# Optimization experiments

Measured on AMD Instinct MI355X. Metric: run time of the kernel, lower is better.

Reference implementation:

```python
import jax, jax.numpy as jnp
import numpy as np

T, IO, H, M = 8192, 32, 256, 4  # timesteps, io_width, hidden_width, max ponder steps
EPS = 0.01  # ACT halting epsilon


def setup_inputs() -> dict:
    key = jax.random.key(0)
    ks = jax.random.split(key, 8)
    sc = 0.05
    return {
        "x": jax.random.normal(ks[0], (T, IO), jnp.float32),
        "h0": jnp.zeros((H,), jnp.float32),                       # act1_h initial state
        "Wp": jax.random.normal(ks[1], (H, IO), jnp.float32) * sc,  # input_processing Linear
        "bp": jnp.zeros((H,), jnp.float32),
        "Wx": jax.random.normal(ks[2], (H, H + 1), jnp.float32) * sc,  # ACT cell input weights (+1 first-step flag)
        "Ws": jax.random.normal(ks[3], (H, H), jnp.float32) * sc,      # ACT cell recurrent weights
        "b": jnp.zeros((H,), jnp.float32),
        "wh": jax.random.normal(ks[4], (H,), jnp.float32) * sc,        # halting unit
        "bh": jnp.float32(1.0),
        "Wo": jax.random.normal(ks[5], (IO, H), jnp.float32) * sc,     # ACT output projection
        "bo": jnp.zeros((IO,), jnp.float32),
    }


def reference(x, h0, Wp, bp, Wx, Ws, b, wh, bh, Wo, bo):
    # Faithful translation: per-timestep loop (lax.scan) over the sequence; each step
    # runs input_processing then an ACT (Graves) ponder loop with max M=4 steps.
    # io_noise is identity in eval mode. attention_beam_width=1 => line == current point.
    T_ = x.shape[0]

    def step(carry, x_t):
        h, pc = carry
        lin1 = Wp @ x_t + bp  # [H]
        s = h
        cum = jnp.float32(0.0)
        acc_s = jnp.zeros_like(h)
        acc_y = jnp.zeros_like(bo)
        n_up = jnp.float32(0.0)
        rem = jnp.float32(0.0)
        still = jnp.bool_(True)
        for n in range(M):  # fixed small ponder loop, masked ACT halting
            flag = jnp.full((1,), 1.0 if n == 0 else 0.0, lin1.dtype)
            inp = jnp.concatenate([lin1, flag])  # [H+1]
            s = jnp.tanh(Wx @ inp + Ws @ s + b)
            p = jax.nn.sigmoid(wh @ s + bh)
            halt = (cum + p > 1.0 - EPS) | (n == M - 1)
            w = jnp.where(still, jnp.where(halt, 1.0 - cum, p), 0.0)
            acc_s = acc_s + w * s
            acc_y = acc_y + w * (Wo @ s + bo)
            rem = rem + jnp.where(still & halt, 1.0 - cum, 0.0)
            n_up = n_up + jnp.where(still, 1.0, 0.0)
            cum = cum + w
            still = still & jnp.logical_not(halt)
        ponder = n_up + rem  # N(t) + R(t)
        pc = (pc + ponder) / jnp.float32(T_)  # matches the in-loop division in the original forward
        return (acc_s, pc), acc_y

    (_, pc), ys = jax.lax.scan(step, (h0, jnp.float32(0.0)), x)
    return ys, pc
```

## Files before the change

### kernel.cpp

```cpp
#include <hip/hip_runtime.h>


#define T_  8192
#define IO_ 32
#define H_  256

typedef __attribute__((ext_vector_type(2))) float v2f;

template<int CTRL>
__device__ __forceinline__ float dpp_addf(float x) {
    int xi = __builtin_bit_cast(int, x);
    int d = __builtin_amdgcn_update_dpp(xi, xi, CTRL, 0xF, 0xF, false);
    return x + __builtin_bit_cast(float, d);
}
template<int CTRL>
__device__ __forceinline__ float dpp_get(float x) {
    int xi = __builtin_bit_cast(int, x);
    int d = __builtin_amdgcn_update_dpp(xi, xi, CTRL, 0xF, 0xF, false);
    return __builtin_bit_cast(float, d);
}
__device__ __forceinline__ void bar_lds() {
    asm volatile("s_waitcnt lgkmcnt(0)\n\ts_barrier" ::: "memory");
    __builtin_amdgcn_sched_barrier(0);
}

__device__ __forceinline__ float mv_reduce(const v2f (&wt)[8][8], const v2f (&sc)[8]) {
    float v[8];
    #pragma unroll
    for (int k = 0; k < 8; ++k) {
        v2f a = wt[k][0] * sc[0];
        #pragma unroll
        for (int q = 1; q < 8; ++q) a += wt[k][q] * sc[q];
        v[k] = a.x + a.y;
    }
    #pragma unroll
    for (int k = 0; k < 8; ++k) v[k] = dpp_addf<0x128>(v[k]);
    v[0] += dpp_get<0x124>(v[4]);
    v[1] += dpp_get<0x124>(v[5]);
    v[2] += dpp_get<0x124>(v[6]);
    v[3] += dpp_get<0x124>(v[7]);
    v[0] += dpp_get<0x121>(v[1]);
    v[0] += dpp_get<0x122>(v[2]);
    v[0] += dpp_get<0x123>(v[3]);
    return v[0];
}

__global__ void k_prep(const float* __restrict__ Wx,
                       const float* __restrict__ Wp,
                       const float* __restrict__ bp,
                       const float* __restrict__ b,
                       float* __restrict__ WxpT, float* __restrict__ cvec) {
    int h = blockIdx.x;
    int t = threadIdx.x;
    __shared__ float wxrow[H_];
    for (int j = t; j < H_; j += 64) wxrow[j] = Wx[h * (H_ + 1) + j];
    __syncthreads();
    if (t < IO_) {
        float acc = 0.0f;
        for (int j = 0; j < H_; ++j) acc += wxrow[j] * Wp[j * IO_ + t];
        WxpT[t * H_ + h] = acc;
    } else if (t == IO_) {
        float acc = b[h];
        for (int j = 0; j < H_; ++j) acc += wxrow[j] * bp[j];
        cvec[h] = acc;
    }
}

__global__ void k_u(const float* __restrict__ x,
                    const float* __restrict__ WxpT,
                    const float* __restrict__ cvec,
                    float* __restrict__ U) {
    int t0 = blockIdx.x * 8;
    int tid = threadIdx.x;
    __shared__ float xsf[8 * IO_];
    xsf[tid] = x[(size_t)t0 * IO_ + tid];
    __syncthreads();
    int h = tid;
    float base = cvec[h];
    const float L2E2 = 2.8853900817779268f;
    for (int tt = 0; tt < 8; ++tt) {
        float acc = base;
        #pragma unroll
        for (int io = 0; io < IO_; ++io)
            acc += WxpT[io * H_ + h] * xsf[tt * IO_ + io];
        U[(size_t)(t0 + tt) * H_ + h] = acc * L2E2;
    }
}

__global__ __launch_bounds__(512, 2) void act_chain(
    const float* __restrict__ Ws,
    const float* __restrict__ Wx,
    const float* __restrict__ wh,
    const float* __restrict__ bh1,
    const float* __restrict__ h0,
    float* __restrict__ UAcc,
    float* __restrict__ cumArr,
    float* __restrict__ pc_out)
{
    __shared__ __align__(16) float sbuf[2][320];
    __shared__ __align__(16) float plds[2][8];

    const int tid = threadIdx.x;
    const int w   = tid >> 6;
    const int l   = tid & 63;
    const int m   = l & 15;
    const int rbase = w * 32 + ((l >> 4) & 3) * 8;
    const int r_own = rbase + (m & 7);
    const int swidx = (r_own >> 4) * 20 + (r_own & 15);
    const bool pub  = (l & 8) == 0;

    const float L2E  = 1.4426950408889634f;
    const float L2E2 = 2.8853900817779268f;

    v2f wt[8][8];
    #pragma unroll
    for (int k = 0; k < 8; ++k) {
        const int rk = rbase + ((k + m) & 7);
        const float4* s4 = (const float4*)(Ws + (size_t)rk * H_ + m * 16);
        #pragma unroll
        for (int q = 0; q < 4; ++q) {
            float4 f = s4[q];
            wt[k][2 * q]     = (v2f){f.x * L2E2, f.y * L2E2};
            wt[k][2 * q + 1] = (v2f){f.z * L2E2, f.w * L2E2};
        }
    }

    const float wlf = Wx[(size_t)r_own * (H_ + 1) + H_] * L2E2;
    const float whp = wh[r_own] * (-L2E);
    const float bhp = -bh1[0] * L2E;
    const float thresh = 0.99f;

    float zh;
    {
        v2f sc[8];
        const float4* hp = (const float4*)(h0 + m * 16);
        #pragma unroll
        for (int q = 0; q < 4; ++q) {
            float4 f = hp[q];
            sc[2 * q]     = (v2f){f.x, f.y};
            sc[2 * q + 1] = (v2f){f.z, f.w};
        }
        zh = mv_reduce(wt, sc);
    }

    float pc = 0.0f;
    float un_cur = UAcc[r_own];
    float u0_cur = un_cur + wlf;

    auto round = [&](int WB, int PP, float in, float& z, float& p) -> float {
        float e = __builtin_amdgcn_exp2f(in);
        float s = __builtin_fmaf(-2.0f, __builtin_amdgcn_rcpf(e + 1.0f), 1.0f);
        if (pub) sbuf[WB][swidx] = s;
        float part = whp * s;
        part = dpp_addf<0x121>(part);
        part = dpp_addf<0x122>(part);
        part = dpp_addf<0x124>(part);
        part = dpp_addf<0x142>(part);
        part = dpp_addf<0x143>(part);
        if (l == 63) plds[PP][w] = part;
        bar_lds();
        const float4* sp = (const float4*)(&sbuf[WB][m * 20]);
        float4 f0 = sp[0], f1 = sp[1], f2 = sp[2], f3 = sp[3];
        const float4* pr = (const float4*)(&plds[PP][0]);
        float4 qa = pr[0], qb = pr[1];
        v2f sc[8] = {{f0.x, f0.y}, {f0.z, f0.w}, {f1.x, f1.y}, {f1.z, f1.w},
                     {f2.x, f2.y}, {f2.z, f2.w}, {f3.x, f3.y}, {f3.z, f3.w}};
        z = mv_reduce(wt, sc);
        float dot = ((qa.x + qa.y) + (qa.z + qa.w)) +
                    ((qb.x + qb.y) + (qb.z + qb.w));
        p = __builtin_amdgcn_rcpf(1.0f + __builtin_amdgcn_exp2f(dot + bhp));
        return s;
    };

    #pragma unroll 1
    for (int t = 0; t < T_; ++t) {
        const int tn = (t + 1 < T_) ? t + 1 : t;
        const float un_nxt = UAcc[(size_t)tn * H_ + r_own];

        float z0, p0, z1, p1;
        float s0 = round(0, 0, zh + u0_cur, z0, p0);
        float s1 = round(1, 1, z0 + un_cur, z1, p1);

        bool  halt0  = p0 > thresh;
        float w0     = halt0 ? 1.0f : p0;
        bool  still1 = !halt0;
        float cum1   = w0;
        bool  halt1  = (cum1 + p1 > thresh);
        float w1     = still1 ? (halt1 ? 1.0f - cum1 : p1) : 0.0f;
        float accs   = __builtin_fmaf(w1, s1, w0 * s0);
        float zacc   = __builtin_fmaf(w1, z1, w0 * z0);
        float cum    = cum1 + w1;
        float nup    = still1 ? 2.0f : 1.0f;
        float rem    = halt0 ? 1.0f : (halt1 ? 1.0f - cum1 : 0.0f);

        if (still1 && !halt1) {
            float z2, p2, z3, p3;
            float s2 = round(0, 0, z1 + un_cur, z2, p2);
            bool  halt2 = (cum + p2 > thresh);
            float w2    = halt2 ? 1.0f - cum : p2;
            float rem2  = halt2 ? 1.0f - cum : 0.0f;
            accs = __builtin_fmaf(w2, s2, accs);
            zacc = __builtin_fmaf(w2, z2, zacc);
            float cum3  = cum + w2;
            bool  still3 = !halt2;
            float s3 = round(1, 1, z2 + un_cur, z3, p3);
            float w3 = still3 ? (1.0f - cum3) : 0.0f;
            accs = __builtin_fmaf(w3, s3, accs);
            zacc = __builtin_fmaf(w3, z3, zacc);
            rem  = rem2 + w3;
            cum  = cum3 + w3;
            nup  = still3 ? 4.0f : 3.0f;
        }

        pc = (pc + nup + rem) * (1.0f / (float)T_);
        zh = zacc;
        if (pub) UAcc[(size_t)t * H_ + r_own] = accs;
        if (tid == 0) cumArr[t] = cum;
        un_cur = un_nxt;
        u0_cur = un_nxt + wlf;
    }
    if (tid == 0) pc_out[0] = pc;
}

__global__ void k_out(const float* __restrict__ AccS,
                      const float* __restrict__ Wo,
                      const float* __restrict__ bo,
                      const float* __restrict__ cumArr,
                      float* __restrict__ ys) {
    int t0 = blockIdx.x * 8;
    int tid = threadIdx.x;
    __shared__ float wo[IO_ * 257];
    __shared__ float as[8 * 260];
    for (int i = tid; i < IO_ * H_; i += 256) {
        int o = i / H_, h = i % H_;
        wo[o * 257 + h] = Wo[i];
    }
    for (int i = tid; i < 8 * H_; i += 256) {
        int tt = i / H_, h = i % H_;
        as[tt * 260 + h] = AccS[(size_t)t0 * H_ + i];
    }
    __syncthreads();
    int tt = tid >> 5, o = tid & 31;
    float acc = cumArr[t0 + tt] * bo[o];
    #pragma unroll 4
    for (int h = 0; h < H_; ++h) acc += wo[o * 257 + h] * as[tt * 260 + h];
    ys[(size_t)(t0 + tt) * IO_ + o] = acc;
}

extern "C" void kernel_launch(void* const* d_in, const int* in_sizes, int n_in,
                              void* d_out, int out_size, void* d_ws, size_t ws_size,
                              hipStream_t stream) {
    const float* x  = (const float*)d_in[0];
    const float* h0 = (const float*)d_in[1];
    const float* Wp = (const float*)d_in[2];
    const float* bp = (const float*)d_in[3];
    const float* Wx = (const float*)d_in[4];
    const float* Ws = (const float*)d_in[5];
    const float* b  = (const float*)d_in[6];
    const float* wh = (const float*)d_in[7];
    const float* bh = (const float*)d_in[8];
    const float* Wo = (const float*)d_in[9];
    const float* bo = (const float*)d_in[10];
    float* out = (float*)d_out;

    char* ws = (char*)d_ws;
    float* WxpT = (float*)ws;
    float* cvec = (float*)(ws + 32768);
    float* cumA = (float*)(ws + 33792);
    float* UAcc = (float*)(ws + 66560);

    k_prep<<<H_, 64, 0, stream>>>(Wx, Wp, bp, b, WxpT, cvec);
    k_u<<<T_ / 8, 256, 0, stream>>>(x, WxpT, cvec, UAcc);
    act_chain<<<1, 512, 0, stream>>>(Ws, Wx, wh, bh, h0, UAcc, cumA,
                                     out + (size_t)T_ * IO_);
    k_out<<<T_ / 8, 256, 0, stream>>>(UAcc, Wo, bo, cumA, out);
}
```

Before: 12.87 ms.

## Remap recurrent matvec to 2 rows x 4 column-chunks per lane

Changes how the Ws recurrent matvec is split across the 512 threads. Each lane now holds two full rows over a 64-column chunk, four lanes cover a row, and the reduction needs only two DPP adds instead of the 8-row rotated layout with a longer DPP tree. Each lane reads its 64 state values straight from LDS as float4s. This aims to shorten the reduction on the serial per-step critical path, at the cost of 64 LDS floats per lane per round instead of 16, a different padding layout, and a pair of tanh values computed per lane.

Result: faster. 12.00 ms (-6.8%).

```diff
diff --git a/kernel.cpp b/kernel.cpp
--- a/kernel.cpp
+++ b/kernel.cpp
@@ -13,36 +13,9 @@
     int d = __builtin_amdgcn_update_dpp(xi, xi, CTRL, 0xF, 0xF, false);
     return x + __builtin_bit_cast(float, d);
 }
-template<int CTRL>
-__device__ __forceinline__ float dpp_get(float x) {
-    int xi = __builtin_bit_cast(int, x);
-    int d = __builtin_amdgcn_update_dpp(xi, xi, CTRL, 0xF, 0xF, false);
-    return __builtin_bit_cast(float, d);
-}
 __device__ __forceinline__ void bar_lds() {
     asm volatile("s_waitcnt lgkmcnt(0)\n\ts_barrier" ::: "memory");
     __builtin_amdgcn_sched_barrier(0);
-}
-
-__device__ __forceinline__ float mv_reduce(const v2f (&wt)[8][8], const v2f (&sc)[8]) {
-    float v[8];
-    #pragma unroll
-    for (int k = 0; k < 8; ++k) {
-        v2f a = wt[k][0] * sc[0];
-        #pragma unroll
-        for (int q = 1; q < 8; ++q) a += wt[k][q] * sc[q];
-        v[k] = a.x + a.y;
-    }
-    #pragma unroll
-    for (int k = 0; k < 8; ++k) v[k] = dpp_addf<0x128>(v[k]);
-    v[0] += dpp_get<0x124>(v[4]);
-    v[1] += dpp_get<0x124>(v[5]);
-    v[2] += dpp_get<0x124>(v[6]);
-    v[3] += dpp_get<0x124>(v[7]);
-    v[0] += dpp_get<0x121>(v[1]);
-    v[0] += dpp_get<0x122>(v[2]);
-    v[0] += dpp_get<0x123>(v[3]);
-    return v[0];
 }
 
 __global__ void k_prep(const float* __restrict__ Wx,
@@ -97,89 +70,105 @@
     float* __restrict__ cumArr,
     float* __restrict__ pc_out)
 {
-    __shared__ __align__(16) float sbuf[2][320];
+    __shared__ __align__(16) float sbuf[2][4 * 68];
     __shared__ __align__(16) float plds[2][8];
 
     const int tid = threadIdx.x;
     const int w   = tid >> 6;
     const int l   = tid & 63;
-    const int m   = l & 15;
-    const int rbase = w * 32 + ((l >> 4) & 3) * 8;
-    const int r_own = rbase + (m & 7);
-    const int swidx = (r_own >> 4) * 20 + (r_own & 15);
-    const bool pub  = (l & 8) == 0;
+    const int rg  = l >> 2;
+    const int c   = l & 3;
+    const int rowbase = w * 32 + rg * 2;
+    const int schunk  = rowbase >> 6;
+    const int soff    = rowbase & 63;
 
     const float L2E  = 1.4426950408889634f;
     const float L2E2 = 2.8853900817779268f;
 
-    v2f wt[8][8];
+    v2f wt[2][32];
     #pragma unroll
-    for (int k = 0; k < 8; ++k) {
-        const int rk = rbase + ((k + m) & 7);
-        const float4* s4 = (const float4*)(Ws + (size_t)rk * H_ + m * 16);
-        #pragma unroll
-        for (int q = 0; q < 4; ++q) {
-            float4 f = s4[q];
-            wt[k][2 * q]     = (v2f){f.x * L2E2, f.y * L2E2};
-            wt[k][2 * q + 1] = (v2f){f.z * L2E2, f.w * L2E2};
+    for (int r = 0; r < 2; ++r) {
+        const float4* src = (const float4*)(Ws + (size_t)(rowbase + r) * H_ + c * 64);
+        #pragma unroll
+        for (int q = 0; q < 16; ++q) {
+            float4 f = src[q];
+            wt[r][2 * q]     = (v2f){f.x * L2E2, f.y * L2E2};
+            wt[r][2 * q + 1] = (v2f){f.z * L2E2, f.w * L2E2};
         }
     }
 
-    const float wlf = Wx[(size_t)r_own * (H_ + 1) + H_] * L2E2;
-    const float whp = wh[r_own] * (-L2E);
+    v2f wl2, whp2;
+    wl2.x  = Wx[(size_t)rowbase * (H_ + 1) + H_] * L2E2;
+    wl2.y  = Wx[(size_t)(rowbase + 1) * (H_ + 1) + H_] * L2E2;
+    whp2.x = wh[rowbase]     * (-L2E);
+    whp2.y = wh[rowbase + 1] * (-L2E);
     const float bhp = -bh1[0] * L2E;
-    const float thresh = 0.99f;
-
-    float zh;
+    const float thresh = 1.0f - 0.01f;
+
+    auto matvec = [&](const float4* sp) -> v2f {
+        v2f a0a = {0.f, 0.f}, a0b = {0.f, 0.f};
+        v2f a1a = {0.f, 0.f}, a1b = {0.f, 0.f};
+        #pragma unroll
+        for (int q = 0; q < 16; ++q) {
+            float4 f = sp[q];
+            v2f sa = (v2f){f.x, f.y};
+            v2f sb = (v2f){f.z, f.w};
+            a0a = a0a + wt[0][2 * q]     * sa;
+            a0b = a0b + wt[0][2 * q + 1] * sb;
+            a1a = a1a + wt[1][2 * q]     * sa;
+            a1b = a1b + wt[1][2 * q + 1] * sb;
+        }
+        v2f t0 = a0a + a0b, t1 = a1a + a1b;
+        float y0 = t0.x + t0.y;
+        float y1 = t1.x + t1.y;
+        y0 = dpp_addf<0xB1>(y0); y0 = dpp_addf<0x4E>(y0);
+        y1 = dpp_addf<0xB1>(y1); y1 = dpp_addf<0x4E>(y1);
+        return (v2f){y0, y1};
+    };
+
+    v2f zh;
     {
-        v2f sc[8];
-        const float4* hp = (const float4*)(h0 + m * 16);
-        #pragma unroll
-        for (int q = 0; q < 4; ++q) {
-            float4 f = hp[q];
-            sc[2 * q]     = (v2f){f.x, f.y};
-            sc[2 * q + 1] = (v2f){f.z, f.w};
-        }
-        zh = mv_reduce(wt, sc);
+        float4 hbuf[16];
+        const float4* hp = (const float4*)(h0 + c * 64);
+        #pragma unroll
+        for (int q = 0; q < 16; ++q) hbuf[q] = hp[q];
+        zh = matvec(hbuf);
     }
 
     float pc = 0.0f;
-    float un_cur = UAcc[r_own];
-    float u0_cur = un_cur + wlf;
-
-    auto round = [&](int WB, int PP, float in, float& z, float& p) -> float {
-        float e = __builtin_amdgcn_exp2f(in);
-        float s = __builtin_fmaf(-2.0f, __builtin_amdgcn_rcpf(e + 1.0f), 1.0f);
-        if (pub) sbuf[WB][swidx] = s;
-        float part = whp * s;
-        part = dpp_addf<0x121>(part);
-        part = dpp_addf<0x122>(part);
+    v2f un = *(const v2f*)(UAcc + rowbase);
+
+    auto round = [&](int WB, int PP, v2f in, v2f& z, float& p) -> v2f {
+        float e0 = __builtin_amdgcn_exp2f(in.x);
+        float e1 = __builtin_amdgcn_exp2f(in.y);
+        float s0 = __builtin_fmaf(-2.0f, __builtin_amdgcn_rcpf(e0 + 1.0f), 1.0f);
+        float s1 = __builtin_fmaf(-2.0f, __builtin_amdgcn_rcpf(e1 + 1.0f), 1.0f);
+        if (c == 0) *(v2f*)(&sbuf[WB][schunk * 68 + soff]) = (v2f){s0, s1};
+        float part = __builtin_fmaf(whp2.x, s0, whp2.y * s1);
         part = dpp_addf<0x124>(part);
+        part = dpp_addf<0x128>(part);
         part = dpp_addf<0x142>(part);
         part = dpp_addf<0x143>(part);
         if (l == 63) plds[PP][w] = part;
         bar_lds();
-        const float4* sp = (const float4*)(&sbuf[WB][m * 20]);
-        float4 f0 = sp[0], f1 = sp[1], f2 = sp[2], f3 = sp[3];
-        const float4* pr = (const float4*)(&plds[PP][0]);
-        float4 qa = pr[0], qb = pr[1];
-        v2f sc[8] = {{f0.x, f0.y}, {f0.z, f0.w}, {f1.x, f1.y}, {f1.z, f1.w},
-                     {f2.x, f2.y}, {f2.z, f2.w}, {f3.x, f3.y}, {f3.z, f3.w}};
-        z = mv_reduce(wt, sc);
-        float dot = ((qa.x + qa.y) + (qa.z + qa.w)) +
-                    ((qb.x + qb.y) + (qb.z + qb.w));
+        z = matvec((const float4*)(&sbuf[WB][c * 68]));
+        float4 pa = *(const float4*)(&plds[PP][0]);
+        float4 pb = *(const float4*)(&plds[PP][4]);
+        float dot = ((pa.x + pa.y) + (pa.z + pa.w)) +
+                    ((pb.x + pb.y) + (pb.z + pb.w));
         p = __builtin_amdgcn_rcpf(1.0f + __builtin_amdgcn_exp2f(dot + bhp));
-        return s;
+        return (v2f){s0, s1};
     };
 
     #pragma unroll 1
     for (int t = 0; t < T_; ++t) {
         const int tn = (t + 1 < T_) ? t + 1 : t;
-        const float un_nxt = UAcc[(size_t)tn * H_ + r_own];
-
-        float z0, p0, z1, p1;
-        float s0 = round(0, 0, zh + u0_cur, z0, p0);
-        float s1 = round(1, 1, z0 + un_cur, z1, p1);
+        const v2f un_nxt = *(const v2f*)(UAcc + (size_t)tn * H_ + rowbase);
+
+        v2f z0, z1;
+        float p0, p1;
+        v2f s0 = round(0, 0, zh + un + wl2, z0, p0);
+        v2f s1 = round(1, 1, z0 + un,       z1, p1);
 
         bool  halt0  = p0 > thresh;
         float w0     = halt0 ? 1.0f : p0;
@@ -187,26 +176,27 @@
         float cum1   = w0;
         bool  halt1  = (cum1 + p1 > thresh);
         float w1     = still1 ? (halt1 ? 1.0f - cum1 : p1) : 0.0f;
-        float accs   = __builtin_fmaf(w1, s1, w0 * s0);
-        float zacc   = __builtin_fmaf(w1, z1, w0 * z0);
+        v2f   accs   = w0 * s0 + w1 * s1;
+        v2f   zacc   = w0 * z0 + w1 * z1;
         float cum    = cum1 + w1;
         float nup    = still1 ? 2.0f : 1.0f;
         float rem    = halt0 ? 1.0f : (halt1 ? 1.0f - cum1 : 0.0f);
 
         if (still1 && !halt1) {
-            float z2, p2, z3, p3;
-            float s2 = round(0, 0, z1 + un_cur, z2, p2);
+            v2f z2, z3;
+            float p2, p3;
+            v2f s2 = round(0, 0, z1 + un, z2, p2);
             bool  halt2 = (cum + p2 > thresh);
             float w2    = halt2 ? 1.0f - cum : p2;
             float rem2  = halt2 ? 1.0f - cum : 0.0f;
-            accs = __builtin_fmaf(w2, s2, accs);
-            zacc = __builtin_fmaf(w2, z2, zacc);
-            float cum3  = cum + w2;
+            accs = accs + w2 * s2;
+            zacc = zacc + w2 * z2;
+            float cum3   = cum + w2;
             bool  still3 = !halt2;
-            float s3 = round(1, 1, z2 + un_cur, z3, p3);
+            v2f s3 = round(1, 1, z2 + un, z3, p3);
             float w3 = still3 ? (1.0f - cum3) : 0.0f;
-            accs = __builtin_fmaf(w3, s3, accs);
-            zacc = __builtin_fmaf(w3, z3, zacc);
+            accs = accs + w3 * s3;
+            zacc = zacc + w3 * z3;
             rem  = rem2 + w3;
             cum  = cum3 + w3;
             nup  = still3 ? 4.0f : 3.0f;
@@ -214,10 +204,9 @@
 
         pc = (pc + nup + rem) * (1.0f / (float)T_);
         zh = zacc;
-        if (pub) UAcc[(size_t)t * H_ + r_own] = accs;
+        if (c == 0) *(v2f*)(UAcc + (size_t)t * H_ + rowbase) = accs;
         if (tid == 0) cumArr[t] = cum;
-        un_cur = un_nxt;
-        u0_cur = un_nxt + wlf;
+        un = un_nxt;
     }
     if (tid == 0) pc_out[0] = pc;
 }
```
